# Kernel optimization log

Measured on AMD Instinct MI355X. Metric: run time of the kernel, lower is better.

## Reference

```python
import jax, jax.numpy as jnp
import numpy as np

D_MODEL = 1024
N_HEADS = 16
D_HEAD = D_MODEL // N_HEADS
WINDOW = 256
ATTN_SCALE = 1.0
SCALE = float(np.sqrt(D_HEAD))
NEG = -10000.0


def setup_inputs() -> dict:
    key = jax.random.key(0)
    ks = jax.random.split(key, 7)
    B, S = 2, 2048
    q = jax.random.normal(ks[0], (B, S, D_MODEL), dtype=jnp.float32)
    k = jax.random.normal(ks[1], (B, S, D_MODEL), dtype=jnp.float32)
    v = jax.random.normal(ks[2], (B, S, D_MODEL), dtype=jnp.float32)
    # Xavier-uniform-like scale for square linear weights: sqrt(6/(fan_in+fan_out))
    lim = float(np.sqrt(6.0 / (D_MODEL + D_MODEL)))
    def xavier(kk):
        return jax.random.uniform(kk, (D_MODEL, D_MODEL), minval=-lim, maxval=lim, dtype=jnp.float32)
    return {"q": q, "k": k, "v": v,
            "WQ": xavier(ks[3]), "WK": xavier(ks[4]),
            "WV": xavier(ks[5]), "WO": xavier(ks[6])}


def _split_heads(x):
    B, S, _ = x.shape
    return x.reshape(B, S, N_HEADS, D_HEAD).transpose(0, 2, 1, 3)  # [B,H,S,Dh]


def reference(q, k, v, WQ, WK, WV, WO):
    B, Sq, _ = q.shape
    Sk = k.shape[1]
    # torch nn.Linear: y = x @ W.T
    qh = _split_heads(q @ WQ.T) / SCALE          # [B,H,Sq,Dh]
    kh = _split_heads(k @ WK.T)                  # [B,H,Sk,Dh]
    vh = _split_heads(v @ WV.T)                  # [B,H,Sk,Dh]
    scores = jnp.einsum('bhqd,bhkd->bhqk', qh, kh) * ATTN_SCALE
    # global abs-max normalization (clamped at 1)
    scores = scores / jnp.maximum(jnp.max(jnp.abs(scores)), 1.0)
    # sliding window mask: key j visible to query i iff i-WINDOW+1 <= j <= i
    qi = jnp.arange(Sq)[:, None]
    kj = jnp.arange(Sk)[None, :]
    win = (kj <= qi) & (kj > qi - WINDOW)        # [Sq,Sk] bool
    scores = jnp.where(win[None, None], scores, NEG)
    attn = jax.nn.softmax(scores, axis=-1)
    out = jnp.einsum('bhqk,bhkd->bhqd', attn, vh)
    out = out.transpose(0, 2, 1, 3).reshape(B, Sq, D_MODEL)
    out = out @ WO.T
    out = out / jnp.maximum(jnp.mean(jnp.abs(out)), 1.0)
    return out
```

## Files before the change

kernel.cpp:

```cpp
#include <hip/hip_runtime.h>
#include <hip/hip_bf16.h>

#define S_LEN 2048
#define DM    1024
#define NH    16
#define DH    64
#define WIN   256
#define BATCH 2

using f32x4   = __attribute__((ext_vector_type(4))) float;
using bf16x8  = __attribute__((ext_vector_type(8))) short;
using ushort8 = __attribute__((ext_vector_type(8))) unsigned short;

static __device__ __forceinline__ unsigned short f2bf(float f) {
  unsigned int x = __float_as_uint(f);
  x += 0x7fffu + ((x >> 16) & 1u);
  return (unsigned short)(x >> 16);
}

typedef const __attribute__((address_space(1))) void* gas_t;
typedef __attribute__((address_space(3))) void* las_t;
static __device__ __forceinline__ void gload16(const void* g, void* l) {
  __builtin_amdgcn_global_load_lds((gas_t)g, (las_t)l, 16, 0, 0);
}

__global__ void k_init(unsigned int* absmax) { *absmax = 0u; }

__global__ __launch_bounds__(256) void k_cvt4(const float* __restrict__ w0,
                                              const float* __restrict__ w1,
                                              const float* __restrict__ w2,
                                              const float* __restrict__ w3,
                                              unsigned short* __restrict__ dst) {
  const float* src = (blockIdx.z == 0) ? w0 : (blockIdx.z == 1) ? w1 : (blockIdx.z == 2) ? w2 : w3;
  unsigned short* d = dst + (size_t)blockIdx.z * DM * DM;
  const int n4 = (DM * DM) / 4;
  int i = blockIdx.x * blockDim.x + threadIdx.x;
  int stride = gridDim.x * blockDim.x;
  for (; i < n4; i += stride) {
    float4 f = ((const float4*)src)[i];
    ushort4 o;
    o.x = f2bf(f.x); o.y = f2bf(f.y); o.z = f2bf(f.z); o.w = f2bf(f.w);
    ((ushort4*)d)[i] = o;
  }
}

__global__ __launch_bounds__(256) void k_cvt_in(const float* __restrict__ q,
                                                const float* __restrict__ k,
                                                const float* __restrict__ v,
                                                unsigned short* __restrict__ qb,
                                                unsigned short* __restrict__ kb,
                                                unsigned short* __restrict__ vb) {
  const float* src = (blockIdx.z == 0) ? q : (blockIdx.z == 1) ? k : v;
  unsigned short* dst = (blockIdx.z == 0) ? qb : (blockIdx.z == 1) ? kb : vb;
  const int n8 = (BATCH * S_LEN * DM) / 8;
  int i = blockIdx.x * blockDim.x + threadIdx.x;
  int stride = gridDim.x * blockDim.x;
  for (; i < n8; i += stride) {
    float4 f0 = ((const float4*)src)[2 * i];
    float4 f1 = ((const float4*)src)[2 * i + 1];
    ushort8 u;
    u[0] = f2bf(f0.x); u[1] = f2bf(f0.y); u[2] = f2bf(f0.z); u[3] = f2bf(f0.w);
    u[4] = f2bf(f1.x); u[5] = f2bf(f1.y); u[6] = f2bf(f1.z); u[7] = f2bf(f1.w);
    ((ushort8*)dst)[i] = u;
  }
}

__device__ __forceinline__ void gemm128_core(const unsigned short* __restrict__ A,
                                             const unsigned short* __restrict__ Bw,
                                             void* __restrict__ Cptr, float oscale, int omode,
                                             int R0, int C0) {
  __shared__ unsigned short As[128][64];
  __shared__ unsigned short Bs[128][64];
  const int tid = threadIdx.x, lane = tid & 63, w = tid >> 6;
  const int wr = w >> 1, wc = w & 1;

  int srow[4], scol[4];
#pragma unroll
  for (int c = 0; c < 4; ++c) {
    srow[c] = c * 32 + w * 8 + (lane >> 3);
    scol[c] = ((lane & 7) ^ (srow[c] & 7)) << 3;
  }

  f32x4 z = {0.f, 0.f, 0.f, 0.f};
  f32x4 acc[4][4];
#pragma unroll
  for (int i = 0; i < 4; ++i)
#pragma unroll
    for (int j = 0; j < 4; ++j) acc[i][j] = z;

  unsigned short* Af = &As[0][0];
  unsigned short* Bf = &Bs[0][0];
  const int cb = 16 * (lane >> 4);

  for (int k0 = 0; k0 < DM; k0 += 64) {
#pragma unroll
    for (int c = 0; c < 4; ++c) {
      gload16(A  + (size_t)(R0 + srow[c]) * DM + k0 + scol[c], Af + c * 2048 + w * 512);
      gload16(Bw + (size_t)(C0 + srow[c]) * DM + k0 + scol[c], Bf + c * 2048 + w * 512);
    }
    __syncthreads();

    bf16x8 av[4][2], bv[4][2];
#pragma unroll
    for (int i = 0; i < 4; ++i) {
      int row = 64 * wr + 16 * i + (lane & 15);
      int sw = (row & 7) << 4;
      const char* rp = (const char*)Af + row * 128;
      av[i][0] = *(const bf16x8*)(rp + (cb ^ sw));
      av[i][1] = *(const bf16x8*)(rp + ((cb + 64) ^ sw));
    }
#pragma unroll
    for (int j = 0; j < 4; ++j) {
      int row = 64 * wc + 16 * j + (lane & 15);
      int sw = (row & 7) << 4;
      const char* rp = (const char*)Bf + row * 128;
      bv[j][0] = *(const bf16x8*)(rp + (cb ^ sw));
      bv[j][1] = *(const bf16x8*)(rp + ((cb + 64) ^ sw));
    }
#pragma unroll
    for (int i = 0; i < 4; ++i)
#pragma unroll
      for (int j = 0; j < 4; ++j) {
        acc[i][j] = __builtin_amdgcn_mfma_f32_16x16x32_bf16(av[i][0], bv[j][0], acc[i][j], 0, 0, 0);
        acc[i][j] = __builtin_amdgcn_mfma_f32_16x16x32_bf16(av[i][1], bv[j][1], acc[i][j], 0, 0, 0);
      }
    __syncthreads();
  }

#pragma unroll
  for (int i = 0; i < 4; ++i) {
#pragma unroll
    for (int j = 0; j < 4; ++j) {
#pragma unroll
      for (int r = 0; r < 4; ++r) {
        int grow = R0 + 64 * wr + 16 * i + 4 * (lane >> 4) + r;
        int gcol = C0 + 64 * wc + 16 * j + (lane & 15);
        float vv = acc[i][j][r] * oscale;
        if (omode == 0) {
          ((float*)Cptr)[(size_t)grow * DM + gcol] = vv;
        } else {
          int b = grow >> 11, s = grow & (S_LEN - 1);
          int h = gcol >> 6, d = gcol & 63;
          if (omode == 1)
            ((unsigned short*)Cptr)[(((size_t)(b * NH + h) * S_LEN + s) << 6) + d] = f2bf(vv);
          else
            ((unsigned short*)Cptr)[(((size_t)(b * NH + h) * DH + d) << 11) + s] = f2bf(vv);
        }
      }
    }
  }
}

__global__ __launch_bounds__(256) void k_gemm_qkv(const unsigned short* __restrict__ qb,
                                                  const unsigned short* __restrict__ kb,
                                                  const unsigned short* __restrict__ vb,
                                                  const unsigned short* __restrict__ WbQ,
                                                  const unsigned short* __restrict__ WbK,
                                                  const unsigned short* __restrict__ WbV,
                                                  unsigned short* __restrict__ qh,
                                                  unsigned short* __restrict__ kh,
                                                  unsigned short* __restrict__ vt) {
  const unsigned short* A; const unsigned short* B; void* C; float sc; int om;
  if (blockIdx.z == 0)      { A = qb; B = WbQ; C = qh; sc = 0.125f; om = 1; }
  else if (blockIdx.z == 1) { A = kb; B = WbK; C = kh; sc = 1.0f;   om = 1; }
  else                      { A = vb; B = WbV; C = vt; sc = 1.0f;   om = 2; }
  gemm128_core(A, B, C, sc, om, blockIdx.x * 128, blockIdx.y * 128);
}

__global__ __launch_bounds__(256) void k_gemm_out(const unsigned short* __restrict__ A,
                                                  const unsigned short* __restrict__ Bw,
                                                  float* __restrict__ C) {
  gemm128_core(A, Bw, C, 1.0f, 0, blockIdx.x * 128, blockIdx.y * 128);
}

__global__ __launch_bounds__(256) void k_scoresmax(const unsigned short* __restrict__ qh,
                                                   const unsigned short* __restrict__ kh,
                                                   unsigned int* __restrict__ absmax) {
  __shared__ unsigned short Ks[128][64];
  const int tid = threadIdx.x, lane = tid & 63, w = tid >> 6;
  const size_t base = (size_t)blockIdx.y * S_LEN * DH;
  const unsigned short* Q = qh + base;
  const unsigned short* K = kh + base;
  const int q0 = blockIdx.x * 128;

  bf16x8 a[2][2];
#pragma unroll
  for (int rb = 0; rb < 2; ++rb) {
    const unsigned short* qr = Q + (size_t)(q0 + 32 * w + 16 * rb + (lane & 15)) * DH + 8 * (lane >> 4);
    a[rb][0] = *(const bf16x8*)qr;
    a[rb][1] = *(const bf16x8*)(qr + 32);
  }

  int srow[4], scol[4];
#pragma unroll
  for (int c = 0; c < 4; ++c) {
    srow[c] = c * 32 + w * 8 + (lane >> 3);
    scol[c] = ((lane & 7) ^ (srow[c] & 7)) << 3;
  }
  unsigned short* Kf = &Ks[0][0];
  const int cbb = 16 * (lane >> 4);

  float m = 0.f;
  for (int kc = 0; kc < S_LEN; kc += 128) {
    __syncthreads();
#pragma unroll
    for (int c = 0; c < 4; ++c)
      gload16(K + (size_t)(kc + srow[c]) * DH + scol[c], Kf + c * 2048 + w * 512);
    __syncthreads();
#pragma unroll
    for (int cb = 0; cb < 8; ++cb) {
      int row = 16 * cb + (lane & 15);
      int sw = (row & 7) << 4;
      const char* rp = (const char*)Kf + row * 128;
      bf16x8 b0 = *(const bf16x8*)(rp + (cbb ^ sw));
      bf16x8 b1 = *(const bf16x8*)(rp + ((cbb + 64) ^ sw));
#pragma unroll
      for (int rb = 0; rb < 2; ++rb) {
        f32x4 acc = {0.f, 0.f, 0.f, 0.f};
        acc = __builtin_amdgcn_mfma_f32_16x16x32_bf16(a[rb][0], b0, acc, 0, 0, 0);
        acc = __builtin_amdgcn_mfma_f32_16x16x32_bf16(a[rb][1], b1, acc, 0, 0, 0);
        m = fmaxf(m, fmaxf(fmaxf(fabsf(acc[0]), fabsf(acc[1])), fmaxf(fabsf(acc[2]), fabsf(acc[3]))));
      }
    }
  }
#pragma unroll
  for (int mk = 1; mk < 64; mk <<= 1) m = fmaxf(m, __shfl_xor(m, mk, 64));
  __shared__ float red[4];
  if (lane == 0) red[w] = m;
  __syncthreads();
  if (threadIdx.x == 0)
    atomicMax(absmax, __float_as_uint(fmaxf(fmaxf(red[0], red[1]), fmaxf(red[2], red[3]))));
}

#define NT 10
__global__ __launch_bounds__(256) void k_attn(const unsigned short* __restrict__ qh,
                                              const unsigned short* __restrict__ kh,
                                              const unsigned short* __restrict__ vt,
                                              const unsigned int* __restrict__ absmax,
                                              unsigned short* __restrict__ attn_c) {
  __shared__ unsigned short Ks[2][32][72];
  __shared__ unsigned short Vts[2][64][40];
  __shared__ unsigned short Pl[4][16][40];
  const int tid = threadIdx.x, lane = tid & 63, w = tid >> 6;
  const int bh = blockIdx.y, b = bh >> 4, h = bh & 15;
  const int Q0 = blockIdx.x * 64;
  const int kstart = Q0 - WIN;
  const size_t base = (size_t)bh * S_LEN * DH;
  const unsigned short* Kb = kh + base;
  const unsigned short* Vtb = vt + base;

  const int skrow = tid >> 3, skcol = (tid & 7) << 3;
  const int svd = tid >> 2, svcol = (tid & 3) << 3;

  const float invM = 1.0f / fmaxf(__uint_as_float(*absmax), 1.0f);
  const unsigned short* Qp = qh + base + (size_t)(Q0 + 16 * w + (lane & 15)) * DH + 8 * (lane >> 4);
  bf16x8 a0 = *(const bf16x8*)Qp;
  bf16x8 a1 = *(const bf16x8*)(Qp + 32);

  ushort8 rk, rv;
  ushort8 zz = {0, 0, 0, 0, 0, 0, 0, 0};
#define LOADT(T) do {                                                        \
    int kk = kstart + 32 * (T) + skrow;                                      \
    rk = (kk >= 0) ? *(const ushort8*)(Kb + (size_t)kk * DH + skcol) : zz;   \
    int kc = kstart + 32 * (T) + svcol;                                      \
    rv = (kc >= 0) ? *(const ushort8*)(Vtb + (size_t)svd * S_LEN + kc) : zz; \
  } while (0)
#define WRITET(buf) do {                                                     \
    *(ushort8*)&Ks[buf][skrow][skcol] = rk;                                  \
    *(ushort8*)&Vts[buf][svd][svcol] = rv;                                   \
  } while (0)

  LOADT(0);
  WRITET(0);
  __syncthreads();

  const int Tlo = w >> 1, Thi = (w >> 1) + 8;
  const int qrow = Q0 + 16 * w + 4 * (lane >> 4);
  float sm[4] = {0.f, 0.f, 0.f, 0.f};
  f32x4 z = {0.f, 0.f, 0.f, 0.f};
  f32x4 o[4];
#pragma unroll
  for (int i = 0; i < 4; ++i) o[i] = z;

  for (int T = 0; T < NT; ++T) {
    const int cur = T & 1;
    const bool act = (T >= Tlo) && (T <= Thi);
    if (T + 1 < NT) LOADT(T + 1);
    if (act) {
      f32x4 p[2];
#pragma unroll
      for (int cb = 0; cb < 2; ++cb) {
        const unsigned short* kr = &Ks[cur][16 * cb + (lane & 15)][8 * (lane >> 4)];
        bf16x8 b0 = *(const bf16x8*)kr;
        bf16x8 b1 = *(const bf16x8*)(kr + 32);
        f32x4 a = z;
        a = __builtin_amdgcn_mfma_f32_16x16x32_bf16(a0, b0, a, 0, 0, 0);
        a = __builtin_amdgcn_mfma_f32_16x16x32_bf16(a1, b1, a, 0, 0, 0);
        p[cb] = a;
      }
#pragma unroll
      for (int cb = 0; cb < 2; ++cb) {
        int kcol = kstart + 32 * T + 16 * cb + (lane & 15);
#pragma unroll
        for (int r = 0; r < 4; ++r) {
          int qq = qrow + r;
          bool ok = (kcol >= 0) && (kcol <= qq) && (kcol + WIN > qq);
          float e = ok ? __expf(p[cb][r] * invM) : 0.f;
          sm[r] += e;
          Pl[w][4 * (lane >> 4) + r][16 * cb + (lane & 15)] = f2bf(e);
        }
      }
    }
    __syncthreads();
    if (act) {
      bf16x8 pa = *(const bf16x8*)&Pl[w][lane & 15][8 * (lane >> 4)];
#pragma unroll
      for (int dt = 0; dt < 4; ++dt) {
        bf16x8 bv = *(const bf16x8*)&Vts[cur][16 * dt + (lane & 15)][8 * (lane >> 4)];
        o[dt] = __builtin_amdgcn_mfma_f32_16x16x32_bf16(pa, bv, o[dt], 0, 0, 0);
      }
    }
    if (T + 1 < NT) WRITET((T + 1) & 1);
    __syncthreads();
  }

#pragma unroll
  for (int r = 0; r < 4; ++r) {
#pragma unroll
    for (int mk = 1; mk < 16; mk <<= 1) sm[r] += __shfl_xor(sm[r], mk, 64);
    sm[r] = 1.0f / sm[r];
  }
#pragma unroll
  for (int dt = 0; dt < 4; ++dt) {
#pragma unroll
    for (int r = 0; r < 4; ++r) {
      int qq = qrow + r;
      float val = o[dt][r] * sm[r];
      attn_c[((size_t)(b * S_LEN + qq) << 10) + h * DH + 16 * dt + (lane & 15)] = f2bf(val);
    }
  }
#undef LOADT
#undef WRITET
}

__global__ __launch_bounds__(256) void k_abspart(const float* __restrict__ x,
                                                 float* __restrict__ part, int n4) {
  float s = 0.f;
  for (int i = blockIdx.x * blockDim.x + threadIdx.x; i < n4; i += gridDim.x * blockDim.x) {
    float4 f = ((const float4*)x)[i];
    s += fabsf(f.x) + fabsf(f.y) + fabsf(f.z) + fabsf(f.w);
  }
#pragma unroll
  for (int mk = 1; mk < 64; mk <<= 1) s += __shfl_xor(s, mk, 64);
  __shared__ float red[4];
  if ((threadIdx.x & 63) == 0) red[threadIdx.x >> 6] = s;
  __syncthreads();
  if (threadIdx.x == 0) part[blockIdx.x] = red[0] + red[1] + red[2] + red[3];
}

__global__ __launch_bounds__(256) void k_absfinal(const float* __restrict__ part,
                                                  float* __restrict__ denominv,
                                                  int n, float invcnt) {
  float s = 0.f;
  for (int i = threadIdx.x; i < n; i += 256) s += part[i];
#pragma unroll
  for (int mk = 1; mk < 64; mk <<= 1) s += __shfl_xor(s, mk, 64);
  __shared__ float red[4];
  if ((threadIdx.x & 63) == 0) red[threadIdx.x >> 6] = s;
  __syncthreads();
  if (threadIdx.x == 0) denominv[0] = 1.0f / fmaxf(s * invcnt, 1.0f);
}

__global__ __launch_bounds__(256) void k_scale(float* __restrict__ x,
                                               const float* __restrict__ denominv, int n4) {
  float d = denominv[0];
  for (int i = blockIdx.x * blockDim.x + threadIdx.x; i < n4; i += gridDim.x * blockDim.x) {
    float4 f = ((float4*)x)[i];
    f.x *= d; f.y *= d; f.z *= d; f.w *= d;
    ((float4*)x)[i] = f;
  }
}

extern "C" void kernel_launch(void* const* d_in, const int* in_sizes, int n_in,
                              void* d_out, int out_size, void* d_ws, size_t ws_size,
                              hipStream_t stream) {
  (void)in_sizes; (void)n_in; (void)out_size; (void)ws_size;
  const float* q  = (const float*)d_in[0];
  const float* k  = (const float*)d_in[1];
  const float* v  = (const float*)d_in[2];
  const float* WQ = (const float*)d_in[3];
  const float* WK = (const float*)d_in[4];
  const float* WV = (const float*)d_in[5];
  const float* WO = (const float*)d_in[6];

  const size_t HS = (size_t)BATCH * NH * S_LEN * DH;
  unsigned short* qb     = (unsigned short*)d_ws;
  unsigned short* kb     = qb + HS;
  unsigned short* vb     = kb + HS;
  unsigned short* qh     = vb + HS;
  unsigned short* kh     = qh + HS;
  unsigned short* vt     = kh + HS;
  unsigned short* Wb     = vt + HS;
  char* scal             = (char*)(Wb + 4 * (size_t)DM * DM);
  unsigned int* absmax   = (unsigned int*)scal;
  float* denominv        = (float*)(scal + 4);
  float* partials        = (float*)(scal + 16);
  unsigned short* attn_c = qb;

  unsigned short* WbQ = Wb;
  unsigned short* WbK = Wb + (size_t)DM * DM;
  unsigned short* WbV = Wb + 2 * (size_t)DM * DM;
  unsigned short* WbO = Wb + 3 * (size_t)DM * DM;

  k_init<<<1, 1, 0, stream>>>(absmax);
  k_cvt4<<<dim3(64, 1, 4), 256, 0, stream>>>(WQ, WK, WV, WO, Wb);
  k_cvt_in<<<dim3(512, 1, 3), 256, 0, stream>>>(q, k, v, qb, kb, vb);

  k_gemm_qkv<<<dim3(32, 8, 3), 256, 0, stream>>>(qb, kb, vb, WbQ, WbK, WbV, qh, kh, vt);

  k_scoresmax<<<dim3(16, 32), 256, 0, stream>>>(qh, kh, absmax);
  k_attn<<<dim3(32, 32), 256, 0, stream>>>(qh, kh, vt, absmax, attn_c);

  k_gemm_out<<<dim3(32, 8), 256, 0, stream>>>(attn_c, WbO, (float*)d_out);

  k_abspart<<<1024, 256, 0, stream>>>((const float*)d_out, partials, (int)(HS / 4));
  k_absfinal<<<1, 256, 0, stream>>>(partials, denominv, 1024, 1.0f / (float)HS);
  k_scale<<<1024, 256, 0, stream>>>((float*)d_out, denominv, (int)(HS / 4));
}
```

Before: 156.5 us.

## Double-buffer LDS staging in GEMMs and scores-max, vectorize epilogue stores

Adds a second LDS buffer to the 128x128 GEMM core and the scores-max kernel so the next K-tile's global-to-LDS loads are issued before the current tile's MFMAs. This removes one barrier per iteration and lets load latency overlap compute. It also templates the output mode and swaps the MFMA operand order for row-major outputs, so each lane holds 4 contiguous columns and can write float4 or ushort4 stores instead of scalar stores. The cost is double the LDS per block, which may reduce occupancy.

```diff
diff --git a/kernel.cpp b/kernel.cpp
--- a/kernel.cpp
+++ b/kernel.cpp
@@ -65,12 +65,13 @@
   }
 }
 
+template<int OMODE, bool SWAP>
 __device__ __forceinline__ void gemm128_core(const unsigned short* __restrict__ A,
                                              const unsigned short* __restrict__ Bw,
-                                             void* __restrict__ Cptr, float oscale, int omode,
+                                             void* __restrict__ Cptr, float oscale,
                                              int R0, int C0) {
-  __shared__ unsigned short As[128][64];
-  __shared__ unsigned short Bs[128][64];
+  __shared__ unsigned short As[2][128][64];
+  __shared__ unsigned short Bs[2][128][64];
   const int tid = threadIdx.x, lane = tid & 63, w = tid >> 6;
   const int wr = w >> 1, wc = w & 1;
 
@@ -88,24 +89,35 @@
 #pragma unroll
     for (int j = 0; j < 4; ++j) acc[i][j] = z;
 
-  unsigned short* Af = &As[0][0];
-  unsigned short* Bf = &Bs[0][0];
+  unsigned short* Af0 = &As[0][0][0];
+  unsigned short* Bf0 = &Bs[0][0][0];
   const int cb = 16 * (lane >> 4);
 
-  for (int k0 = 0; k0 < DM; k0 += 64) {
-#pragma unroll
-    for (int c = 0; c < 4; ++c) {
-      gload16(A  + (size_t)(R0 + srow[c]) * DM + k0 + scol[c], Af + c * 2048 + w * 512);
-      gload16(Bw + (size_t)(C0 + srow[c]) * DM + k0 + scol[c], Bf + c * 2048 + w * 512);
-    }
-    __syncthreads();
-
+#define STAGE_G(buf, k0) do {                                                          \
+    unsigned short* Ad = Af0 + (buf) * 8192 + w * 512;                                 \
+    unsigned short* Bd = Bf0 + (buf) * 8192 + w * 512;                                 \
+    _Pragma("unroll")                                                                  \
+    for (int c = 0; c < 4; ++c) {                                                      \
+      gload16(A  + (size_t)(R0 + srow[c]) * DM + (k0) + scol[c], Ad + c * 2048);       \
+      gload16(Bw + (size_t)(C0 + srow[c]) * DM + (k0) + scol[c], Bd + c * 2048);       \
+    }                                                                                  \
+  } while (0)
+
+  STAGE_G(0, 0);
+  __syncthreads();
+
+  for (int t = 0; t < 16; ++t) {
+    const int cur = t & 1;
+    if (t + 1 < 16) STAGE_G(cur ^ 1, (t + 1) * 64);
+
+    const char* Af = (const char*)(Af0 + cur * 8192);
+    const char* Bf = (const char*)(Bf0 + cur * 8192);
     bf16x8 av[4][2], bv[4][2];
 #pragma unroll
     for (int i = 0; i < 4; ++i) {
       int row = 64 * wr + 16 * i + (lane & 15);
       int sw = (row & 7) << 4;
-      const char* rp = (const char*)Af + row * 128;
+      const char* rp = Af + row * 128;
       av[i][0] = *(const bf16x8*)(rp + (cb ^ sw));
       av[i][1] = *(const bf16x8*)(rp + ((cb + 64) ^ sw));
     }
@@ -113,7 +125,7 @@
     for (int j = 0; j < 4; ++j) {
       int row = 64 * wc + 16 * j + (lane & 15);
       int sw = (row & 7) << 4;
-      const char* rp = (const char*)Bf + row * 128;
+      const char* rp = Bf + row * 128;
       bv[j][0] = *(const bf16x8*)(rp + (cb ^ sw));
       bv[j][1] = *(const bf16x8*)(rp + ((cb + 64) ^ sw));
     }
@@ -121,31 +133,44 @@
     for (int i = 0; i < 4; ++i)
 #pragma unroll
       for (int j = 0; j < 4; ++j) {
-        acc[i][j] = __builtin_amdgcn_mfma_f32_16x16x32_bf16(av[i][0], bv[j][0], acc[i][j], 0, 0, 0);
-        acc[i][j] = __builtin_amdgcn_mfma_f32_16x16x32_bf16(av[i][1], bv[j][1], acc[i][j], 0, 0, 0);
+        if (SWAP) {
+          acc[i][j] = __builtin_amdgcn_mfma_f32_16x16x32_bf16(bv[j][0], av[i][0], acc[i][j], 0, 0, 0);
+          acc[i][j] = __builtin_amdgcn_mfma_f32_16x16x32_bf16(bv[j][1], av[i][1], acc[i][j], 0, 0, 0);
+        } else {
+          acc[i][j] = __builtin_amdgcn_mfma_f32_16x16x32_bf16(av[i][0], bv[j][0], acc[i][j], 0, 0, 0);
+          acc[i][j] = __builtin_amdgcn_mfma_f32_16x16x32_bf16(av[i][1], bv[j][1], acc[i][j], 0, 0, 0);
+        }
       }
     __syncthreads();
   }
+#undef STAGE_G
 
 #pragma unroll
   for (int i = 0; i < 4; ++i) {
 #pragma unroll
     for (int j = 0; j < 4; ++j) {
-#pragma unroll
-      for (int r = 0; r < 4; ++r) {
-        int grow = R0 + 64 * wr + 16 * i + 4 * (lane >> 4) + r;
-        int gcol = C0 + 64 * wc + 16 * j + (lane & 15);
-        float vv = acc[i][j][r] * oscale;
-        if (omode == 0) {
-          ((float*)Cptr)[(size_t)grow * DM + gcol] = vv;
+      if (SWAP) {
+        int grow  = R0 + 64 * wr + 16 * i + (lane & 15);
+        int gcol0 = C0 + 64 * wc + 16 * j + 4 * (lane >> 4);
+        if (OMODE == 0) {
+          float4 st = {acc[i][j][0] * oscale, acc[i][j][1] * oscale,
+                       acc[i][j][2] * oscale, acc[i][j][3] * oscale};
+          *(float4*)((float*)Cptr + (size_t)grow * DM + gcol0) = st;
         } else {
           int b = grow >> 11, s = grow & (S_LEN - 1);
-          int h = gcol >> 6, d = gcol & 63;
-          if (omode == 1)
-            ((unsigned short*)Cptr)[(((size_t)(b * NH + h) * S_LEN + s) << 6) + d] = f2bf(vv);
-          else
-            ((unsigned short*)Cptr)[(((size_t)(b * NH + h) * DH + d) << 11) + s] = f2bf(vv);
+          int h = gcol0 >> 6, d0 = gcol0 & 63;
+          ushort4 st = {f2bf(acc[i][j][0] * oscale), f2bf(acc[i][j][1] * oscale),
+                        f2bf(acc[i][j][2] * oscale), f2bf(acc[i][j][3] * oscale)};
+          *(ushort4*)((unsigned short*)Cptr + (((size_t)(b * NH + h) * S_LEN + s) << 6) + d0) = st;
         }
+      } else {
+        int grow0 = R0 + 64 * wr + 16 * i + 4 * (lane >> 4);
+        int gcol  = C0 + 64 * wc + 16 * j + (lane & 15);
+        int b = grow0 >> 11, s0 = grow0 & (S_LEN - 1);
+        int h = gcol >> 6, d = gcol & 63;
+        ushort4 st = {f2bf(acc[i][j][0] * oscale), f2bf(acc[i][j][1] * oscale),
+                      f2bf(acc[i][j][2] * oscale), f2bf(acc[i][j][3] * oscale)};
+        *(ushort4*)((unsigned short*)Cptr + (((size_t)(b * NH + h) * DH + d) << 11) + s0) = st;
       }
     }
   }
@@ -160,23 +185,22 @@
                                                   unsigned short* __restrict__ qh,
                                                   unsigned short* __restrict__ kh,
                                                   unsigned short* __restrict__ vt) {
-  const unsigned short* A; const unsigned short* B; void* C; float sc; int om;
-  if (blockIdx.z == 0)      { A = qb; B = WbQ; C = qh; sc = 0.125f; om = 1; }
-  else if (blockIdx.z == 1) { A = kb; B = WbK; C = kh; sc = 1.0f;   om = 1; }
-  else                      { A = vb; B = WbV; C = vt; sc = 1.0f;   om = 2; }
-  gemm128_core(A, B, C, sc, om, blockIdx.x * 128, blockIdx.y * 128);
+  const int R0 = blockIdx.x * 128, C0 = blockIdx.y * 128;
+  if (blockIdx.z == 0)      gemm128_core<1, true >(qb, WbQ, qh, 0.125f, R0, C0);
+  else if (blockIdx.z == 1) gemm128_core<1, true >(kb, WbK, kh, 1.0f,   R0, C0);
+  else                      gemm128_core<2, false>(vb, WbV, vt, 1.0f,   R0, C0);
 }
 
 __global__ __launch_bounds__(256) void k_gemm_out(const unsigned short* __restrict__ A,
                                                   const unsigned short* __restrict__ Bw,
                                                   float* __restrict__ C) {
-  gemm128_core(A, Bw, C, 1.0f, 0, blockIdx.x * 128, blockIdx.y * 128);
+  gemm128_core<0, true>(A, Bw, C, 1.0f, blockIdx.x * 128, blockIdx.y * 128);
 }
 
 __global__ __launch_bounds__(256) void k_scoresmax(const unsigned short* __restrict__ qh,
                                                    const unsigned short* __restrict__ kh,
                                                    unsigned int* __restrict__ absmax) {
-  __shared__ unsigned short Ks[128][64];
+  __shared__ unsigned short Ks[2][128][64];
   const int tid = threadIdx.x, lane = tid & 63, w = tid >> 6;
   const size_t base = (size_t)blockIdx.y * S_LEN * DH;
   const unsigned short* Q = qh + base;
@@ -197,21 +221,29 @@
     srow[c] = c * 32 + w * 8 + (lane >> 3);
     scol[c] = ((lane & 7) ^ (srow[c] & 7)) << 3;
   }
-  unsigned short* Kf = &Ks[0][0];
+  unsigned short* Kf0 = &Ks[0][0][0];
   const int cbb = 16 * (lane >> 4);
 
+#define STAGE_K(buf, kc) do {                                                          \
+    unsigned short* Kd = Kf0 + (buf) * 8192 + w * 512;                                 \
+    _Pragma("unroll")                                                                  \
+    for (int c = 0; c < 4; ++c)                                                        \
+      gload16(K + (size_t)((kc) + srow[c]) * DH + scol[c], Kd + c * 2048);             \
+  } while (0)
+
+  STAGE_K(0, 0);
+  __syncthreads();
+
   float m = 0.f;
-  for (int kc = 0; kc < S_LEN; kc += 128) {
-    __syncthreads();
-#pragma unroll
-    for (int c = 0; c < 4; ++c)
-      gload16(K + (size_t)(kc + srow[c]) * DH + scol[c], Kf + c * 2048 + w * 512);
-    __syncthreads();
+  for (int t = 0; t < 16; ++t) {
+    const int cur = t & 1;
+    if (t + 1 < 16) STAGE_K(cur ^ 1, (t + 1) * 128);
+    const char* Kf = (const char*)(Kf0 + cur * 8192);
 #pragma unroll
     for (int cb = 0; cb < 8; ++cb) {
       int row = 16 * cb + (lane & 15);
       int sw = (row & 7) << 4;
-      const char* rp = (const char*)Kf + row * 128;
+      const char* rp = Kf + row * 128;
       bf16x8 b0 = *(const bf16x8*)(rp + (cbb ^ sw));
       bf16x8 b1 = *(const bf16x8*)(rp + ((cbb + 64) ^ sw));
 #pragma unroll
@@ -222,7 +254,10 @@
         m = fmaxf(m, fmaxf(fmaxf(fabsf(acc[0]), fabsf(acc[1])), fmaxf(fabsf(acc[2]), fabsf(acc[3]))));
       }
     }
-  }
+    __syncthreads();
+  }
+#undef STAGE_K
+
 #pragma unroll
   for (int mk = 1; mk < 64; mk <<= 1) m = fmaxf(m, __shfl_xor(m, mk, 64));
   __shared__ float red[4];
```

New measurement: 168.4 us. 7.6% more time.
